# Kernel tuning notes

Hardware: AMD Instinct MI355X
Metric: run time of the kernel (lower is better)

Reference implementation:

```python
import jax, jax.numpy as jnp
import numpy as np

TOP_K = 8
SCORE_FUNC = "sigmoid"
ROUTE_NORM = True
ROUTE_SCALE = 2.5


def setup_inputs() -> dict:
    key = jax.random.key(0)
    k1, k2, k3 = jax.random.split(key, 3)
    B, S, H, E = 4, 4096, 2048, 64
    hidden_states = jax.random.normal(k1, (B, S, H), dtype=jnp.float32)
    # nn.Linear default init scale ~ 1/sqrt(H); exact distribution irrelevant for correctness
    gate_w = jax.random.normal(k2, (E, H), dtype=jnp.float32) * (1.0 / np.sqrt(H))
    expert_bias = jax.random.normal(k3, (E,), dtype=jnp.float32) * 0.1
    return {"hidden_states": hidden_states, "expert_bias": expert_bias, "gate_w": gate_w}


def reference(hidden_states, expert_bias, gate_w):
    B, S, H = hidden_states.shape
    x = hidden_states.reshape(-1, H)  # [T, H]
    logits = jnp.einsum("th,eh->te", x, gate_w)  # [T, E]
    if SCORE_FUNC == "sigmoid":
        scores = jax.nn.sigmoid(logits.astype(jnp.float32))
    else:
        scores = jax.nn.softmax(logits.astype(jnp.float32), axis=-1)
    if expert_bias is not None:
        _, selected_experts = jax.lax.top_k(scores + expert_bias[None, :], TOP_K)
        top_scores = jnp.take_along_axis(scores, selected_experts, axis=1)
    else:
        top_scores, selected_experts = jax.lax.top_k(scores, TOP_K)
    if SCORE_FUNC == "sigmoid" and ROUTE_NORM:
        denom = jnp.sum(top_scores, axis=-1, keepdims=True) + 1e-20
        top_scores = top_scores / denom
    top_scores = top_scores * ROUTE_SCALE
    return top_scores, selected_experts
```

## Files before the change

### kernel.cpp

```cpp
#include <hip/hip_runtime.h>
#include <math.h>

#define T_TOTAL 16384
#define HDIM    2048
#define NEXP    64
#define KS      4
#define KSLICE  (HDIM / KS)
#define TM      256
#define BK      32
#define XS_ST   260
#define WS_ST   68

__global__ __launch_bounds__(256, 3)
void router_gemm_kernel(const float* __restrict__ x,
                        const float* __restrict__ w,
                        float* __restrict__ partial)
{
    __shared__ float Xs[BK][XS_ST];
    __shared__ float Ws[BK][WS_ST];

    const int tid = threadIdx.x;
    const int tb  = blockIdx.x & 63;
    const int ks  = blockIdx.x >> 6;
    const int t0  = tb * TM;
    const int k0  = ks * KSLICE;

    const int kq  = tid & 7;
    const int rr  = tid >> 3;

    const int ex8 = (tid & 7) * 8;
    const int ty8 = (tid >> 3) * 8;

    float acc[8][8];
#pragma unroll
    for (int i = 0; i < 8; ++i)
#pragma unroll
        for (int j = 0; j < 8; ++j) acc[i][j] = 0.0f;

    for (int kc = 0; kc < KSLICE; kc += BK) {
        __syncthreads();

        {
            const float* xg = x + (size_t)t0 * HDIM + (k0 + kc) + kq * 4;
#pragma unroll
            for (int p = 0; p < 8; ++p) {
                const int r = p * 32 + rr;
                const float4 v = *(const float4*)(xg + (size_t)r * HDIM);
                Xs[kq * 4 + 0][r] = v.x;
                Xs[kq * 4 + 1][r] = v.y;
                Xs[kq * 4 + 2][r] = v.z;
                Xs[kq * 4 + 3][r] = v.w;
            }
        }
        {
            const float* wg = w + (k0 + kc) + kq * 4;
#pragma unroll
            for (int p = 0; p < 2; ++p) {
                const int e = p * 32 + rr;
                const float4 v = *(const float4*)(wg + (size_t)e * HDIM);
                Ws[kq * 4 + 0][e] = v.x;
                Ws[kq * 4 + 1][e] = v.y;
                Ws[kq * 4 + 2][e] = v.z;
                Ws[kq * 4 + 3][e] = v.w;
            }
        }
        __syncthreads();

#pragma unroll 4
        for (int k = 0; k < BK; ++k) {
            float xv[8], wv[8];
            *(float4*)&xv[0] = *(const float4*)&Xs[k][ty8];
            *(float4*)&xv[4] = *(const float4*)&Xs[k][ty8 + 4];
            *(float4*)&wv[0] = *(const float4*)&Ws[k][ex8];
            *(float4*)&wv[4] = *(const float4*)&Ws[k][ex8 + 4];
#pragma unroll
            for (int i = 0; i < 8; ++i)
#pragma unroll
                for (int j = 0; j < 8; ++j)
                    acc[i][j] = fmaf(xv[i], wv[j], acc[i][j]);
        }
    }

    float* pp = partial + ((size_t)ks * T_TOTAL + t0) * NEXP;
#pragma unroll
    for (int i = 0; i < 8; ++i) {
        const int t = ty8 + i;
        const float4 s0 = make_float4(acc[i][0], acc[i][1], acc[i][2], acc[i][3]);
        const float4 s1 = make_float4(acc[i][4], acc[i][5], acc[i][6], acc[i][7]);
        *(float4*)(pp + (size_t)t * NEXP + ex8)     = s0;
        *(float4*)(pp + (size_t)t * NEXP + ex8 + 4) = s1;
    }
}

__global__ __launch_bounds__(256)
void router_topk_kernel(const float* __restrict__ partial,
                        const float* __restrict__ bias,
                        float* __restrict__ out_scores,
                        float* __restrict__ out_idx)
{
    const int gid   = blockIdx.x * 256 + threadIdx.x;
    const int token = gid >> 6;
    const int lane  = threadIdx.x & 63;
    if (token >= T_TOTAL) return;

    const size_t base = (size_t)token * NEXP + lane;
    const size_t sl   = (size_t)T_TOTAL * NEXP;
    const float logit = partial[base] + partial[sl + base] +
                        partial[2 * sl + base] + partial[3 * sl + base];

    const float score = 1.0f / (1.0f + expf(-logit));
    float key = score + bias[lane];

    float myscore = 0.0f;
    int   myidx   = 0;
    float denom   = 0.0f;

#pragma unroll
    for (int r = 0; r < 8; ++r) {
        float bk = key;
        int   bi = lane;
#pragma unroll
        for (int off = 32; off > 0; off >>= 1) {
            const float ok = __shfl_xor(bk, off);
            const int   oi = __shfl_xor(bi, off);
            if (ok > bk || (ok == bk && oi < bi)) { bk = ok; bi = oi; }
        }
        const float wsc = __shfl(score, bi);
        denom += wsc;
        if (lane == r)  { myscore = wsc; myidx = bi; }
        if (lane == bi) key = -__builtin_inff();
    }

    const float factor = 2.5f / (denom + 1e-20f);
    if (lane < 8) {
        out_scores[(size_t)token * 8 + lane] = myscore * factor;
        out_idx  [(size_t)token * 8 + lane] = (float)myidx;
    }
}

extern "C" void kernel_launch(void* const* d_in, const int* in_sizes, int n_in,
                              void* d_out, int out_size, void* d_ws, size_t ws_size,
                              hipStream_t stream)
{
    const float* x    = (const float*)d_in[0];
    const float* bias = (const float*)d_in[1];
    const float* w    = (const float*)d_in[2];

    float* out     = (float*)d_out;
    float* partial = (float*)d_ws;

    router_gemm_kernel<<<dim3(64 * KS), dim3(256), 0, stream>>>(x, w, partial);
    router_topk_kernel<<<dim3(T_TOTAL * 64 / 256), dim3(256), 0, stream>>>(
        partial, bias, out, out + (size_t)T_TOTAL * 8);
}
```

Baseline: 252.0 us.

## Drop LDS staging, load operands directly from global, raise split-K count

The GEMM kernel no longer stages X and W tiles in shared memory. Each thread now reads its 8 token rows and 8 expert rows straight from global memory as float4 vectors along K, so the kernel has no barriers. The split-K factor rises to 16 or 8 when the workspace allows, which launches more blocks for occupancy. The partial layout becomes token-major so the top-k kernel can sum a variable number of slices. The cost is poor cross-thread reuse: the same X and W data is reloaded by several threads through cache, and the workspace traffic grows with the larger split.

```diff
diff --git a/kernel.cpp b/kernel.cpp
--- a/kernel.cpp
+++ b/kernel.cpp
@@ -4,32 +4,34 @@
 #define T_TOTAL 16384
 #define HDIM    2048
 #define NEXP    64
-#define KS      4
-#define KSLICE  (HDIM / KS)
-#define TM      256
-#define BK      32
-#define XS_ST   260
-#define WS_ST   68
 
-__global__ __launch_bounds__(256, 3)
+template<int KS>
+__global__ __launch_bounds__(256)
 void router_gemm_kernel(const float* __restrict__ x,
                         const float* __restrict__ w,
                         float* __restrict__ partial)
 {
-    __shared__ float Xs[BK][XS_ST];
-    __shared__ float Ws[BK][WS_ST];
+    constexpr int KSLICE = HDIM / KS;
 
     const int tid = threadIdx.x;
     const int tb  = blockIdx.x & 63;
     const int ks  = blockIdx.x >> 6;
-    const int t0  = tb * TM;
+    const int t0  = tb * 256;
     const int k0  = ks * KSLICE;
 
-    const int kq  = tid & 7;
-    const int rr  = tid >> 3;
+    const int tg  = tid >> 3;
+    const int eg  = tid & 7;
 
-    const int ex8 = (tid & 7) * 8;
-    const int ty8 = (tid >> 3) * 8;
+    const float* xp[8];
+    const float* wp[8];
+    {
+        const float* xb = x + (size_t)(t0 + tg * 8) * HDIM + k0;
+        const float* wb = w + (size_t)(eg * 8) * HDIM + k0;
+#pragma unroll
+        for (int i = 0; i < 8; ++i) xp[i] = xb + (size_t)i * HDIM;
+#pragma unroll
+        for (int j = 0; j < 8; ++j) wp[j] = wb + (size_t)j * HDIM;
+    }
 
     float acc[8][8];
 #pragma unroll
@@ -37,58 +39,30 @@
 #pragma unroll
         for (int j = 0; j < 8; ++j) acc[i][j] = 0.0f;
 
-    for (int kc = 0; kc < KSLICE; kc += BK) {
-        __syncthreads();
-
-        {
-            const float* xg = x + (size_t)t0 * HDIM + (k0 + kc) + kq * 4;
+#pragma unroll 1
+    for (int kc = 0; kc < KSLICE; kc += 4) {
+        float4 xv[8], wv[8];
 #pragma unroll
-            for (int p = 0; p < 8; ++p) {
-                const int r = p * 32 + rr;
-                const float4 v = *(const float4*)(xg + (size_t)r * HDIM);
-                Xs[kq * 4 + 0][r] = v.x;
-                Xs[kq * 4 + 1][r] = v.y;
-                Xs[kq * 4 + 2][r] = v.z;
-                Xs[kq * 4 + 3][r] = v.w;
+        for (int i = 0; i < 8; ++i) xv[i] = *(const float4*)(xp[i] + kc);
+#pragma unroll
+        for (int j = 0; j < 8; ++j) wv[j] = *(const float4*)(wp[j] + kc);
+#pragma unroll
+        for (int i = 0; i < 8; ++i)
+#pragma unroll
+            for (int j = 0; j < 8; ++j) {
+                acc[i][j] = fmaf(xv[i].x, wv[j].x, acc[i][j]);
+                acc[i][j] = fmaf(xv[i].y, wv[j].y, acc[i][j]);
+                acc[i][j] = fmaf(xv[i].z, wv[j].z, acc[i][j]);
+                acc[i][j] = fmaf(xv[i].w, wv[j].w, acc[i][j]);
             }
-        }
-        {
-            const float* wg = w + (k0 + kc) + kq * 4;
-#pragma unroll
-            for (int p = 0; p < 2; ++p) {
-                const int e = p * 32 + rr;
-                const float4 v = *(const float4*)(wg + (size_t)e * HDIM);
-                Ws[kq * 4 + 0][e] = v.x;
-                Ws[kq * 4 + 1][e] = v.y;
-                Ws[kq * 4 + 2][e] = v.z;
-                Ws[kq * 4 + 3][e] = v.w;
-            }
-        }
-        __syncthreads();
-
-#pragma unroll 4
-        for (int k = 0; k < BK; ++k) {
-            float xv[8], wv[8];
-            *(float4*)&xv[0] = *(const float4*)&Xs[k][ty8];
-            *(float4*)&xv[4] = *(const float4*)&Xs[k][ty8 + 4];
-            *(float4*)&wv[0] = *(const float4*)&Ws[k][ex8];
-            *(float4*)&wv[4] = *(const float4*)&Ws[k][ex8 + 4];
-#pragma unroll
-            for (int i = 0; i < 8; ++i)
-#pragma unroll
-                for (int j = 0; j < 8; ++j)
-                    acc[i][j] = fmaf(xv[i], wv[j], acc[i][j]);
-        }
     }
 
-    float* pp = partial + ((size_t)ks * T_TOTAL + t0) * NEXP;
+    float* pp = partial + ((size_t)(t0 + tg * 8) * KS + ks) * NEXP + eg * 8;
 #pragma unroll
     for (int i = 0; i < 8; ++i) {
-        const int t = ty8 + i;
-        const float4 s0 = make_float4(acc[i][0], acc[i][1], acc[i][2], acc[i][3]);
-        const float4 s1 = make_float4(acc[i][4], acc[i][5], acc[i][6], acc[i][7]);
-        *(float4*)(pp + (size_t)t * NEXP + ex8)     = s0;
-        *(float4*)(pp + (size_t)t * NEXP + ex8 + 4) = s1;
+        float* q = pp + (size_t)i * KS * NEXP;
+        *(float4*)(q)     = make_float4(acc[i][0], acc[i][1], acc[i][2], acc[i][3]);
+        *(float4*)(q + 4) = make_float4(acc[i][4], acc[i][5], acc[i][6], acc[i][7]);
     }
 }
 
@@ -96,17 +70,15 @@
 void router_topk_kernel(const float* __restrict__ partial,
                         const float* __restrict__ bias,
                         float* __restrict__ out_scores,
-                        float* __restrict__ out_idx)
+                        float* __restrict__ out_idx,
+                        int ksCount)
 {
-    const int gid   = blockIdx.x * 256 + threadIdx.x;
-    const int token = gid >> 6;
+    const int token = blockIdx.x * 4 + (threadIdx.x >> 6);
     const int lane  = threadIdx.x & 63;
-    if (token >= T_TOTAL) return;
 
-    const size_t base = (size_t)token * NEXP + lane;
-    const size_t sl   = (size_t)T_TOTAL * NEXP;
-    const float logit = partial[base] + partial[sl + base] +
-                        partial[2 * sl + base] + partial[3 * sl + base];
+    const float* pt = partial + (size_t)token * ksCount * NEXP + lane;
+    float logit = 0.0f;
+    for (int s = 0; s < ksCount; ++s) logit += pt[(size_t)s * NEXP];
 
     const float score = 1.0f / (1.0f + expf(-logit));
     float key = score + bias[lane];
@@ -149,7 +121,19 @@
     float* out     = (float*)d_out;
     float* partial = (float*)d_ws;
 
-    router_gemm_kernel<<<dim3(64 * KS), dim3(256), 0, stream>>>(x, w, partial);
-    router_topk_kernel<<<dim3(T_TOTAL * 64 / 256), dim3(256), 0, stream>>>(
-        partial, bias, out, out + (size_t)T_TOTAL * 8);
+    const size_t bytesPerSlice = (size_t)T_TOTAL * NEXP * 4;
+    int ksCount;
+    if (ws_size >= 16 * bytesPerSlice) {
+        ksCount = 16;
+        router_gemm_kernel<16><<<dim3(64 * 16), dim3(256), 0, stream>>>(x, w, partial);
+    } else if (ws_size >= 8 * bytesPerSlice) {
+        ksCount = 8;
+        router_gemm_kernel<8><<<dim3(64 * 8), dim3(256), 0, stream>>>(x, w, partial);
+    } else {
+        ksCount = 4;
+        router_gemm_kernel<4><<<dim3(64 * 4), dim3(256), 0, stream>>>(x, w, partial);
+    }
+
+    router_topk_kernel<<<dim3(T_TOTAL / 4), dim3(256), 0, stream>>>(
+        partial, bias, out, out + (size_t)T_TOTAL * 8, ksCount);
 }
```

Result: slower. 348.2 us (+38.2%).
